# Kernel optimization log

Hardware: AMD Instinct MI355X
Metric: run time of the kernel (lower is better)

## Reference

```python
import jax, jax.numpy as jnp
import numpy as np

N = 50000   # nodes per graph
E = 800000  # edges per graph
D = 128     # in_dim (num_features)
H = 128     # hidden_channels
R = 8       # num_etypes


def setup_inputs() -> dict:
    key = jax.random.key(0)
    ks = jax.random.split(key, 32)
    inp = {}
    inp["x1"] = jax.random.normal(ks[0], (N, D), dtype=jnp.float32)
    inp["edge_index1"] = jax.random.randint(ks[1], (2, E), 0, N)
    inp["edge_type1"] = jnp.sort(jax.random.randint(ks[2], (E,), 0, R))
    inp["x2"] = jax.random.normal(ks[3], (N, D), dtype=jnp.float32)
    inp["edge_index2"] = jax.random.randint(ks[4], (2, E), 0, N)
    inp["edge_type2"] = jnp.sort(jax.random.randint(ks[5], (E,), 0, R))
    # RGCNConv params: relation weights [R, in, out], root weight [in, out], bias [out]
    dims = [(D, H), (H, H), (H, H)]
    k = 6
    for l, (di, do) in enumerate(dims):
        s = 1.0 / np.sqrt(di)
        inp[f"W{l}"] = jax.random.normal(ks[k], (R, di, do), dtype=jnp.float32) * s; k += 1
        inp[f"root{l}"] = jax.random.normal(ks[k], (di, do), dtype=jnp.float32) * s; k += 1
        inp[f"bias{l}"] = jnp.zeros((do,), dtype=jnp.float32)
    # FCL: MLP on concat(u1, u2) of width 2*H -> H -> 1 (assumed architecture)
    s = 1.0 / np.sqrt(2 * H)
    inp["fc1_w"] = jax.random.normal(ks[k], (2 * H, H), dtype=jnp.float32) * s; k += 1
    inp["fc1_b"] = jnp.zeros((H,), dtype=jnp.float32)
    s = 1.0 / np.sqrt(H)
    inp["fc2_w"] = jax.random.normal(ks[k], (H, 1), dtype=jnp.float32) * s; k += 1
    inp["fc2_b"] = jnp.zeros((1,), dtype=jnp.float32)
    return inp


def rgcn_conv(x, src, dst, etype, W, root, bias):
    # PyG RGCNConv: out_i = root @ x_i + bias + sum_r mean_{j in N_r(i)} W_r x_j
    # transform all nodes by all relation weights: [R, N, H]
    t = jnp.einsum('nd,rdh->rnh', x, W)
    msg = t[etype, src]                       # [E, H] per-edge gathered messages
    comb = dst * R + etype                    # combined (node, relation) segment id
    cnt = jax.ops.segment_sum(jnp.ones((E,), x.dtype), comb, num_segments=N * R)
    msg = msg * (1.0 / jnp.maximum(cnt, 1.0))[comb][:, None]  # per-relation mean norm
    agg = jax.ops.segment_sum(msg, dst, num_segments=N)       # scatter-add over relations
    return agg + x @ root + bias


def gnn(x, edge_index, edge_type, params):
    src, dst = edge_index[0], edge_index[1]
    u = jax.nn.relu(rgcn_conv(x, src, dst, edge_type, *params[0]))
    u = jax.nn.relu(rgcn_conv(u, src, dst, edge_type, *params[1]))
    u = rgcn_conv(u, src, dst, edge_type, *params[2])
    return jnp.mean(u, axis=0).reshape(1, -1)  # [1, H]


def reference(x1, edge_index1, edge_type1, x2, edge_index2, edge_type2,
              W0, root0, bias0, W1, root1, bias1, W2, root2, bias2,
              fc1_w, fc1_b, fc2_w, fc2_b):
    params = [(W0, root0, bias0), (W1, root1, bias1), (W2, root2, bias2)]
    u1 = gnn(x1, edge_index1, edge_type1, params)
    u2 = gnn(x2, edge_index2, edge_type2, params)
    h = jnp.concatenate([u1, u2], axis=-1)    # [1, 2H]
    return jax.nn.relu(h @ fc1_w + fc1_b) @ fc2_w + fc2_b  # [1, 1]
```

## Files before the change

### kernel.cpp

```cpp
#include <hip/hip_runtime.h>

#define R_ET 8
#define DH 128

typedef __bf16 bf16x8 __attribute__((ext_vector_type(8)));
typedef float f32x4 __attribute__((ext_vector_type(4)));

__device__ __forceinline__ ushort f2bf(float f) {
  unsigned u = __float_as_uint(f);
  u += 0x7fff + ((u >> 16) & 1);
  return (ushort)(u >> 16);
}


__global__ void count_kernel(const int* __restrict__ ei, const int* __restrict__ et,
                             int* __restrict__ cnt, int E) {
  int e = blockIdx.x * blockDim.x + threadIdx.x;
  if (e < E) atomicAdd(&cnt[ei[E + e] * R_ET + et[e]], 1);
}

__global__ __launch_bounds__(1024) void scan1_kernel(const int* __restrict__ cnt,
                                                     int* __restrict__ off,
                                                     int* __restrict__ bsum, int N) {
  __shared__ int s[1024];
  int tid = threadIdx.x;
  int node = blockIdx.x * 1024 + tid;
  int d = 0;
  if (node < N) {
    const int4* c = (const int4*)&cnt[node * R_ET];
    int4 a = c[0], b = c[1];
    d = a.x + a.y + a.z + a.w + b.x + b.y + b.z + b.w;
  }
  s[tid] = d;
  __syncthreads();
  for (int step = 1; step < 1024; step <<= 1) {
    int v = (tid >= step) ? s[tid - step] : 0;
    __syncthreads();
    s[tid] += v;
    __syncthreads();
  }
  if (node < N) off[node] = s[tid] - d;
  if (tid == 1023) bsum[blockIdx.x] = s[1023];
}

__global__ __launch_bounds__(1024) void scan2_kernel(int* __restrict__ bsum, int nb) {
  __shared__ int s[1024];
  int tid = threadIdx.x;
  int v = (tid < nb) ? bsum[tid] : 0;
  s[tid] = v;
  __syncthreads();
  for (int step = 1; step < 1024; step <<= 1) {
    int x = (tid >= step) ? s[tid - step] : 0;
    __syncthreads();
    s[tid] += x;
    __syncthreads();
  }
  if (tid < nb) bsum[tid] = s[tid] - v;
}

__global__ __launch_bounds__(1024) void scan3_kernel(int* __restrict__ off,
                                                     int* __restrict__ cursor,
                                                     const int* __restrict__ bsum,
                                                     int N, int E) {
  int node = blockIdx.x * 1024 + threadIdx.x;
  if (node < N) {
    int o = off[node] + bsum[blockIdx.x];
    off[node] = o;
    cursor[node] = o;
  }
  if (node == 0) off[N] = E;
}

__global__ void place_kernel(const int* __restrict__ ei, const int* __restrict__ et,
                             const int* __restrict__ cnt, int* __restrict__ cursor,
                             int2* __restrict__ meta, int E) {
  int e = blockIdx.x * blockDim.x + threadIdx.x;
  if (e >= E) return;
  int src = ei[e], dst = ei[E + e], r = et[e];
  int slot = atomicAdd(&cursor[dst], 1);
  meta[slot] = make_int2(src | (r << 28),
                         __float_as_int(1.f / (float)cnt[dst * R_ET + r]));
}

__global__ __launch_bounds__(256) void wconv_kernel(const float* __restrict__ root,
                                                    const float* __restrict__ W,
                                                    ushort* __restrict__ Wt) {
  int mat = blockIdx.x;
  const float* src = (mat == 0) ? root : (W + (size_t)(mat - 1) * DH * DH);
  ushort* dst = Wt + (size_t)mat * DH * DH;
  for (int idx = threadIdx.x; idx < DH * DH; idx += 256) {
    int n = idx >> 7, k = idx & 127;
    dst[n * DH + (((k >> 3) ^ (n & 7)) << 3) + (k & 7)] = f2bf(src[k * DH + n]);
  }
}

__global__ __launch_bounds__(256) void aconv_kernel(const float* __restrict__ src,
                                                    ushort* __restrict__ dst,
                                                    int total, int padtotal) {
  int i4 = (blockIdx.x * 256 + threadIdx.x) * 4;
  if (i4 >= padtotal) return;
  int row = i4 >> 7, k = i4 & 127;
  ushort4 o = make_ushort4(0, 0, 0, 0);
  if (i4 < total) {
    float4 v = *(const float4*)&src[i4];
    o = make_ushort4(f2bf(v.x), f2bf(v.y), f2bf(v.z), f2bf(v.w));
  }
  *(ushort4*)&dst[(size_t)row * DH + (((k >> 3) ^ (row & 7)) << 3) + (k & 7)] = o;
}

__global__ __launch_bounds__(256) void gemm_mfma(
    const ushort* __restrict__ Abf, const ushort* __restrict__ Wt,
    const float* __restrict__ bias, float* __restrict__ y,
    ushort* __restrict__ t, int N) {
  __shared__ ushort As[128 * DH];
  __shared__ ushort Bs[128 * DH];
  const int tid = threadIdx.x;
  const int wave = tid >> 6, lane = tid & 63;
  const int quad = lane >> 4, l15 = lane & 15;
  const int rbase = blockIdx.x * 128;
  const int wr = (wave >> 1) * 64, wc = (wave & 1) * 64;

  const ushort* gA = Abf + (size_t)rbase * DH;
#pragma unroll
  for (int it = 0; it < 8; it++) {
    __builtin_amdgcn_global_load_lds(
        (const __attribute__((address_space(1))) void*)(gA + (it * 256 + tid) * 8),
        (__attribute__((address_space(3))) void*)(As + (it * 256 + wave * 64) * 8), 16, 0, 0);
  }

  for (int m = 0; m < 3; m++) {
    const int mat = blockIdx.y * 3 + m;
    const ushort* gB = Wt + (size_t)mat * DH * DH;
    if (m) __syncthreads();
#pragma unroll
    for (int it = 0; it < 8; it++) {
      __builtin_amdgcn_global_load_lds(
          (const __attribute__((address_space(1))) void*)(gB + (it * 256 + tid) * 8),
          (__attribute__((address_space(3))) void*)(Bs + (it * 256 + wave * 64) * 8), 16, 0, 0);
    }
    __syncthreads();

    f32x4 acc[4][4];
#pragma unroll
    for (int i = 0; i < 4; i++)
#pragma unroll
      for (int j = 0; j < 4; j++) acc[i][j] = (f32x4){0.f, 0.f, 0.f, 0.f};

#pragma unroll
    for (int kc = 0; kc < 4; kc++) {
      bf16x8 af[4], bfr[4];
#pragma unroll
      for (int i = 0; i < 4; i++) {
        int ra = wr + i * 16 + l15;
        int rb = wc + i * 16 + l15;
        af[i] = *(const bf16x8*)&As[ra * DH + (((kc * 4 + quad) ^ (ra & 7)) << 3)];
        bfr[i] = *(const bf16x8*)&Bs[rb * DH + (((kc * 4 + quad) ^ (rb & 7)) << 3)];
      }
#pragma unroll
      for (int i = 0; i < 4; i++)
#pragma unroll
        for (int j = 0; j < 4; j++)
          acc[i][j] = __builtin_amdgcn_mfma_f32_16x16x32_bf16(af[i], bfr[j], acc[i][j], 0, 0, 0);
    }

    if (mat == 0) {
#pragma unroll
      for (int j = 0; j < 4; j++) {
        int col = wc + j * 16 + l15;
        float bv = bias[col];
#pragma unroll
        for (int i = 0; i < 4; i++)
#pragma unroll
          for (int r = 0; r < 4; r++) {
            int row = rbase + wr + i * 16 + quad * 4 + r;
            if (row < N) y[(size_t)row * DH + col] = acc[i][j][r] + bv;
          }
      }
    } else {
      ushort* tp = t + (size_t)(mat - 1) * N * DH;
#pragma unroll
      for (int j = 0; j < 4; j++) {
        int col = wc + j * 16 + l15;
#pragma unroll
        for (int i = 0; i < 4; i++)
#pragma unroll
          for (int r = 0; r < 4; r++) {
            int row = rbase + wr + i * 16 + quad * 4 + r;
            if (row < N) tp[(size_t)row * DH + col] = f2bf(acc[i][j][r]);
          }
      }
    }
  }
}

__device__ __forceinline__ void gather_accum(const int2* __restrict__ meta,
                                             const ushort* __restrict__ t,
                                             int start, int end, int lane, int N,
                                             float& ax, float& ay) {
  const int colb = lane * 2;
  for (int base = start; base < end; base += 64) {
    int m = min(64, end - base);
    int2 md = make_int2(0, 0);
    if (lane < m) md = meta[base + lane];
    int j = 0;
    for (; j + 4 <= m; j += 4) {
      int p0 = __shfl(md.x, j),     q0 = __shfl(md.y, j);
      int p1 = __shfl(md.x, j + 1), q1 = __shfl(md.y, j + 1);
      int p2 = __shfl(md.x, j + 2), q2 = __shfl(md.y, j + 2);
      int p3 = __shfl(md.x, j + 3), q3 = __shfl(md.y, j + 3);
      unsigned u0 = *(const unsigned*)&t[(((size_t)((unsigned)p0 >> 28) * N + (p0 & 0x0fffffff)) << 7) + colb];
      unsigned u1 = *(const unsigned*)&t[(((size_t)((unsigned)p1 >> 28) * N + (p1 & 0x0fffffff)) << 7) + colb];
      unsigned u2 = *(const unsigned*)&t[(((size_t)((unsigned)p2 >> 28) * N + (p2 & 0x0fffffff)) << 7) + colb];
      unsigned u3 = *(const unsigned*)&t[(((size_t)((unsigned)p3 >> 28) * N + (p3 & 0x0fffffff)) << 7) + colb];
      float s0 = __int_as_float(q0), s1 = __int_as_float(q1);
      float s2 = __int_as_float(q2), s3 = __int_as_float(q3);
      ax = fmaf(__uint_as_float(u0 << 16), s0, ax);
      ay = fmaf(__uint_as_float(u0 & 0xffff0000u), s0, ay);
      ax = fmaf(__uint_as_float(u1 << 16), s1, ax);
      ay = fmaf(__uint_as_float(u1 & 0xffff0000u), s1, ay);
      ax = fmaf(__uint_as_float(u2 << 16), s2, ax);
      ay = fmaf(__uint_as_float(u2 & 0xffff0000u), s2, ay);
      ax = fmaf(__uint_as_float(u3 << 16), s3, ax);
      ay = fmaf(__uint_as_float(u3 & 0xffff0000u), s3, ay);
    }
    for (; j < m; j++) {
      int pj = __shfl(md.x, j);
      float sj = __int_as_float(__shfl(md.y, j));
      unsigned u = *(const unsigned*)&t[(((size_t)((unsigned)pj >> 28) * N + (pj & 0x0fffffff)) << 7) + colb];
      ax = fmaf(__uint_as_float(u << 16), sj, ax);
      ay = fmaf(__uint_as_float(u & 0xffff0000u), sj, ay);
    }
  }
}

__global__ __launch_bounds__(256) void gather_mid(
    const int* __restrict__ off, const int2* __restrict__ meta,
    const ushort* __restrict__ t, const float* __restrict__ y,
    ushort* __restrict__ Abf, int N) {
  int dst = blockIdx.x * 4 + (threadIdx.x >> 6);
  if (dst >= N) return;
  int lane = threadIdx.x & 63;
  float ax = 0.f, ay = 0.f;
  gather_accum(meta, t, off[dst], off[dst + 1], lane, N, ax, ay);
  float2 yv = *(const float2*)&y[(size_t)dst * DH + lane * 2];
  float rx = fmaxf(yv.x + ax, 0.f);
  float ry = fmaxf(yv.y + ay, 0.f);
  unsigned o = (unsigned)f2bf(rx) | ((unsigned)f2bf(ry) << 16);
  int k = lane * 2;
  *(unsigned*)&Abf[(size_t)dst * DH + (((k >> 3) ^ (dst & 7)) << 3) + (k & 7)] = o;
}

__global__ __launch_bounds__(256) void gather_last(
    const int* __restrict__ off, const int2* __restrict__ meta,
    const ushort* __restrict__ t, float* __restrict__ y, int N) {
  int dst = blockIdx.x * 4 + (threadIdx.x >> 6);
  if (dst >= N) return;
  int lane = threadIdx.x & 63;
  float ax = 0.f, ay = 0.f;
  gather_accum(meta, t, off[dst], off[dst + 1], lane, N, ax, ay);
  float2* yp = (float2*)&y[(size_t)dst * DH + lane * 2];
  float2 yv = *yp;
  yv.x += ax;
  yv.y += ay;
  *yp = yv;
}

__global__ __launch_bounds__(256) void pool_kernel(const float* __restrict__ y,
                                                   float* __restrict__ u, int N) {
  __shared__ float s[256];
  int tid = threadIdx.x;
  int c = tid & 127, rr = tid >> 7;
  int n0 = blockIdx.x * 100;
  int nend = min(n0 + 100, N);
  float sum = 0.f;
  for (int n = n0 + rr; n < nend; n += 2) sum += y[(size_t)n * DH + c];
  s[tid] = sum;
  __syncthreads();
  if (tid < 128) atomicAdd(&u[c], s[tid] + s[tid + 128]);
}

__global__ __launch_bounds__(256) void mlp_kernel(
    const float* __restrict__ u, const float* __restrict__ fc1w,
    const float* __restrict__ fc1b, const float* __restrict__ fc2w,
    const float* __restrict__ fc2b, float* __restrict__ out, int N) {
  __shared__ float uin[256];
  __shared__ float hred[128];
  int tid = threadIdx.x;
  uin[tid] = u[tid] * (1.f / (float)N);
  __syncthreads();
  if (tid < 128) {
    float s = fc1b[tid];
    for (int i = 0; i < 256; i++) s = fmaf(uin[i], fc1w[i * 128 + tid], s);
    s = fmaxf(s, 0.f);
    hred[tid] = s * fc2w[tid];
  }
  __syncthreads();
  if (tid == 0) {
    float s = fc2b[0];
    for (int i = 0; i < 128; i++) s += hred[i];
    out[0] = s;
  }
}

extern "C" void kernel_launch(void* const* d_in, const int* in_sizes, int n_in,
                              void* d_out, int out_size, void* d_ws, size_t ws_size,
                              hipStream_t stream) {
  const float* x[2] = {(const float*)d_in[0], (const float*)d_in[3]};
  const int* ei[2] = {(const int*)d_in[1], (const int*)d_in[4]};
  const int* et[2] = {(const int*)d_in[2], (const int*)d_in[5]};
  const float* Wp[3] = {(const float*)d_in[6], (const float*)d_in[9], (const float*)d_in[12]};
  const float* rootp[3] = {(const float*)d_in[7], (const float*)d_in[10], (const float*)d_in[13]};
  const float* biasp[3] = {(const float*)d_in[8], (const float*)d_in[11], (const float*)d_in[14]};
  const float* fc1w = (const float*)d_in[15];
  const float* fc1b = (const float*)d_in[16];
  const float* fc2w = (const float*)d_in[17];
  const float* fc2b = (const float*)d_in[18];

  const int N = in_sizes[0] / DH;
  const int E = in_sizes[2];
  const int Npad = (N + 127) & ~127;
  const int NB = (N + 1023) / 1024;

  char* ws = (char*)d_ws;
  size_t ob = 0;
  auto alloc = [&](size_t bytes) {
    void* p = ws + ob;
    ob = (ob + bytes + 255) & ~(size_t)255;
    return p;
  };
  float* y = (float*)alloc((size_t)N * DH * 4);
  int* cnt = (int*)alloc((size_t)N * R_ET * 4);
  int* offs = (int*)alloc((size_t)(N + 1) * 4);
  int* cursor = (int*)alloc((size_t)N * 4);
  int* bsum = (int*)alloc(1024 * 4);
  int2* meta = (int2*)alloc((size_t)E * 8);
  float* u = (float*)alloc(1024);
  ushort* Abf = (ushort*)alloc((size_t)Npad * DH * 2);
  ushort* Wt = (ushort*)alloc((size_t)3 * 9 * DH * DH * 2);
  ushort* tbuf = (ushort*)alloc((size_t)R_ET * N * DH * 2);
  (void)ws_size;

  hipMemsetAsync(u, 0, 2 * DH * sizeof(float), stream);
  for (int l = 0; l < 3; l++)
    wconv_kernel<<<9, 256, 0, stream>>>(rootp[l], Wp[l], Wt + (size_t)l * 9 * DH * DH);

  dim3 ggrid(Npad / 128, 3);
  dim3 egrid((E + 255) / 256);
  dim3 ngrid((N + 3) / 4);
  const int total = N * DH, padtotal = Npad * DH;
  dim3 agrid((padtotal / 4 + 255) / 256);

  for (int g = 0; g < 2; g++) {
    hipMemsetAsync(cnt, 0, (size_t)N * R_ET * sizeof(int), stream);
    count_kernel<<<egrid, 256, 0, stream>>>(ei[g], et[g], cnt, E);
    scan1_kernel<<<NB, 1024, 0, stream>>>(cnt, offs, bsum, N);
    scan2_kernel<<<1, 1024, 0, stream>>>(bsum, NB);
    scan3_kernel<<<NB, 1024, 0, stream>>>(offs, cursor, bsum, N, E);
    place_kernel<<<egrid, 256, 0, stream>>>(ei[g], et[g], cnt, cursor, meta, E);
    aconv_kernel<<<agrid, 256, 0, stream>>>(x[g], Abf, total, padtotal);
    for (int l = 0; l < 3; l++) {
      gemm_mfma<<<ggrid, 256, 0, stream>>>(Abf, Wt + (size_t)l * 9 * DH * DH,
                                           biasp[l], y, tbuf, N);
      if (l < 2) {
        gather_mid<<<ngrid, 256, 0, stream>>>(offs, meta, tbuf, y, Abf, N);
      } else {
        gather_last<<<ngrid, 256, 0, stream>>>(offs, meta, tbuf, y, N);
      }
    }
    pool_kernel<<<(N + 99) / 100, 256, 0, stream>>>(y, u + g * DH, N);
  }
  mlp_kernel<<<1, 256, 0, stream>>>(u, fc1w, fc1b, fc2w, fc2b, (float*)d_out, N);
}
```

Baseline: 889.7 us.

## Swap MFMA operands for vectorized epilogue stores and prefetch next weight tile

Swaps the MFMA A/B operands so each lane holds four consecutive output columns of one node. The epilogue can then write float4 (fp32) and packed 8-byte bf16 stores instead of scalar 4-byte and 2-byte stores. It also issues the next relation weight tile's LDS load right after the MFMA loop, so that load overlaps with the epilogue stores. The goal is to cut store instruction count and uncoalesced write traffic in the transform GEMM, and to hide weight load latency.

```diff
diff --git a/kernel.cpp b/kernel.cpp
--- a/kernel.cpp
+++ b/kernel.cpp
@@ -127,17 +127,18 @@
         (const __attribute__((address_space(1))) void*)(gA + (it * 256 + tid) * 8),
         (__attribute__((address_space(3))) void*)(As + (it * 256 + wave * 64) * 8), 16, 0, 0);
   }
-
-  for (int m = 0; m < 3; m++) {
-    const int mat = blockIdx.y * 3 + m;
-    const ushort* gB = Wt + (size_t)mat * DH * DH;
-    if (m) __syncthreads();
+  {
+    const ushort* gB = Wt + (size_t)(blockIdx.y * 3) * DH * DH;
 #pragma unroll
     for (int it = 0; it < 8; it++) {
       __builtin_amdgcn_global_load_lds(
           (const __attribute__((address_space(1))) void*)(gB + (it * 256 + tid) * 8),
           (__attribute__((address_space(3))) void*)(Bs + (it * 256 + wave * 64) * 8), 16, 0, 0);
     }
+  }
+
+  for (int m = 0; m < 3; m++) {
+    const int mat = blockIdx.y * 3 + m;
     __syncthreads();
 
     f32x4 acc[4][4];
@@ -160,34 +161,49 @@
       for (int i = 0; i < 4; i++)
 #pragma unroll
         for (int j = 0; j < 4; j++)
-          acc[i][j] = __builtin_amdgcn_mfma_f32_16x16x32_bf16(af[i], bfr[j], acc[i][j], 0, 0, 0);
+          acc[i][j] = __builtin_amdgcn_mfma_f32_16x16x32_bf16(bfr[j], af[i], acc[i][j], 0, 0, 0);
+    }
+
+    if (m < 2) {
+      __syncthreads();
+      const ushort* gB = Wt + (size_t)(mat + 1) * DH * DH;
+#pragma unroll
+      for (int it = 0; it < 8; it++) {
+        __builtin_amdgcn_global_load_lds(
+            (const __attribute__((address_space(1))) void*)(gB + (it * 256 + tid) * 8),
+            (__attribute__((address_space(3))) void*)(Bs + (it * 256 + wave * 64) * 8), 16, 0, 0);
+      }
     }
 
     if (mat == 0) {
 #pragma unroll
-      for (int j = 0; j < 4; j++) {
-        int col = wc + j * 16 + l15;
-        float bv = bias[col];
-#pragma unroll
-        for (int i = 0; i < 4; i++)
-#pragma unroll
-          for (int r = 0; r < 4; r++) {
-            int row = rbase + wr + i * 16 + quad * 4 + r;
-            if (row < N) y[(size_t)row * DH + col] = acc[i][j][r] + bv;
+      for (int i = 0; i < 4; i++) {
+        int node = rbase + wr + i * 16 + l15;
+        if (node < N) {
+#pragma unroll
+          for (int j = 0; j < 4; j++) {
+            int c0 = wc + j * 16 + quad * 4;
+            float4 bv = *(const float4*)&bias[c0];
+            float4 v = make_float4(acc[i][j][0] + bv.x, acc[i][j][1] + bv.y,
+                                   acc[i][j][2] + bv.z, acc[i][j][3] + bv.w);
+            *(float4*)&y[(size_t)node * DH + c0] = v;
           }
+        }
       }
     } else {
-      ushort* tp = t + (size_t)(mat - 1) * N * DH;
-#pragma unroll
-      for (int j = 0; j < 4; j++) {
-        int col = wc + j * 16 + l15;
-#pragma unroll
-        for (int i = 0; i < 4; i++)
-#pragma unroll
-          for (int r = 0; r < 4; r++) {
-            int row = rbase + wr + i * 16 + quad * 4 + r;
-            if (row < N) tp[(size_t)row * DH + col] = f2bf(acc[i][j][r]);
+      ushort* tp = t + (size_t)(mat - 1) * (size_t)N * DH;
+#pragma unroll
+      for (int i = 0; i < 4; i++) {
+        int node = rbase + wr + i * 16 + l15;
+        if (node < N) {
+#pragma unroll
+          for (int j = 0; j < 4; j++) {
+            int c0 = wc + j * 16 + quad * 4;
+            unsigned lo = (unsigned)f2bf(acc[i][j][0]) | ((unsigned)f2bf(acc[i][j][1]) << 16);
+            unsigned hi = (unsigned)f2bf(acc[i][j][2]) | ((unsigned)f2bf(acc[i][j][3]) << 16);
+            *(uint2*)&tp[(size_t)node * DH + c0] = make_uint2(lo, hi);
           }
+        }
       }
     }
   }
```

New measurement: 895.7 us. Within noise of the previous version (+0.7%).
